# Kernel tuning notes

Measured on AMD Instinct MI355X. Metric: run time of the kernel, lower is better.

The kernel has to match this reference:

```python
import jax, jax.numpy as jnp
import numpy as np
import math

B, S, E = 2, 2048, 2048
H, KVH = 16, 4
HD = E // H  # 128
ROPE_BASE = 10000.0


def _rope_cos_sin(seq_len, dim, base=ROPE_BASE):
    inv_freq = 1.0 / (base ** (jnp.arange(0, dim, 2, dtype=jnp.float32) / dim))
    t = jnp.arange(seq_len, dtype=jnp.float32)
    freqs = jnp.outer(t, inv_freq)            # [S, dim/2]
    emb = jnp.concatenate([freqs, freqs], -1)  # [S, dim]
    return jnp.cos(emb), jnp.sin(emb)          # each [S, dim]


def _rotate_half(x):
    h = x.shape[-1] // 2
    return jnp.concatenate([-x[..., h:], x[..., :h]], axis=-1)


def setup_inputs() -> dict:
    key = jax.random.key(0)
    ks = jax.random.split(key, 6)
    x = jax.random.normal(ks[0], (B, S, E), dtype=jnp.float32)
    # xavier_uniform for Linear(in, out): weight stored as [out, in] in torch;
    # we store transposed [in, out] for x @ W.
    def xavier(k, fan_in, fan_out):
        a = math.sqrt(6.0 / (fan_in + fan_out))
        return jax.random.uniform(k, (fan_in, fan_out), jnp.float32, -a, a)
    wq = xavier(ks[1], E, H * HD)
    wk = xavier(ks[2], E, KVH * HD)
    wv = xavier(ks[3], E, KVH * HD)
    wo = xavier(ks[4], E, E)
    # causal mask: True above diagonal => masked
    attn_mask = jnp.triu(jnp.ones((S, S), dtype=bool), k=1)
    return {"x": x, "wq": wq, "wk": wk, "wv": wv, "wo": wo, "attn_mask": attn_mask}


def reference(x, wq, wk, wv, wo, attn_mask):
    b, s, _ = x.shape
    q = (x @ wq).reshape(b, s, H, HD).transpose(0, 2, 1, 3)     # [B,H,S,HD]
    k = (x @ wk).reshape(b, s, KVH, HD).transpose(0, 2, 1, 3)   # [B,KVH,S,HD]
    v = (x @ wv).reshape(b, s, KVH, HD).transpose(0, 2, 1, 3)
    cos, sin = _rope_cos_sin(s, HD)
    cos = cos[None, None]  # [1,1,S,HD]
    sin = sin[None, None]
    q = q * cos + _rotate_half(q) * sin
    k = k * cos + _rotate_half(k) * sin
    # repeat KV heads to match Q heads (GQA)
    groups = H // KVH
    k = jnp.repeat(k, groups, axis=1)  # [B,H,S,HD]
    v = jnp.repeat(v, groups, axis=1)
    scale = 1.0 / math.sqrt(HD)
    scores = jnp.einsum('bhqd,bhkd->bhqk', q, k) * scale  # [B,H,S,S]
    scores = jnp.where(attn_mask[None, None], -jnp.inf, scores)
    attn = jax.nn.softmax(scores, axis=-1)
    out = jnp.einsum('bhqk,bhkd->bhqd', attn, v)  # [B,H,S,HD]
    out = out.transpose(0, 2, 1, 3).reshape(b, s, E)
    return out @ wo
```

## Files before the change

kernel.cpp:

```cpp
#include <hip/hip_runtime.h>
#include <math.h>

#define S_LEN 2048
#define EDIM  2048
#define HDIM  128

typedef __attribute__((ext_vector_type(8))) __bf16 bf16x8;
typedef __attribute__((ext_vector_type(4))) __bf16 bf16x4;
typedef __attribute__((ext_vector_type(4))) float  f32x4;

__device__ __forceinline__ f32x4 mfma16x16x32(bf16x8 a, bf16x8 b, f32x4 c) {
  return __builtin_amdgcn_mfma_f32_16x16x32_bf16(a, b, c, 0, 0, 0);
}

__device__ __forceinline__ void gload_lds16(const __bf16* g, __bf16* l) {
  __builtin_amdgcn_global_load_lds(
      (const __attribute__((address_space(1))) void*)g,
      (__attribute__((address_space(3))) void*)l, 16, 0, 0);
}

__global__ void zero_flag(int* f) { *f = 0; }

__global__ void probe_dtype(const unsigned int* __restrict__ x, int* __restrict__ flag) {
  const int tid = threadIdx.x;
  int cnt = 0;
  for (int i = tid; i < 4096; i += 256) {
    unsigned e = (x[i] >> 7) & 0xFFu;
    cnt += (e >= 110u && e <= 135u) ? 1 : 0;
  }
  #pragma unroll
  for (int m = 1; m < 64; m <<= 1) cnt += __shfl_xor(cnt, m, 64);
  if ((tid & 63) == 0) atomicAdd(flag, cnt);
}

__global__ __launch_bounds__(256) void xconv(const void* __restrict__ xv,
                                             __bf16* __restrict__ xb,
                                             const int* __restrict__ flag) {
  const bool bf = (*flag > 2048);
  const size_t base = ((size_t)blockIdx.x * 256 + threadIdx.x) * 8;
  bf16x8 v;
  if (bf) {
    v = *(const bf16x8*)((const __bf16*)xv + base);
  } else {
    const float* xf = (const float*)xv + base;
    float4 f0 = *(const float4*)(xf);
    float4 f1 = *(const float4*)(xf + 4);
    v[0] = (__bf16)f0.x; v[1] = (__bf16)f0.y; v[2] = (__bf16)f0.z; v[3] = (__bf16)f0.w;
    v[4] = (__bf16)f1.x; v[5] = (__bf16)f1.y; v[6] = (__bf16)f1.z; v[7] = (__bf16)f1.w;
  }
  *(bf16x8*)(xb + base) = v;
}

__global__ __launch_bounds__(256) void trans_w(const void* __restrict__ Wv,
                                               __bf16* __restrict__ WT,
                                               int Kd, int Nd,
                                               const int* __restrict__ flag) {
  const bool bf = (*flag > 2048);
  __shared__ __bf16 t[64 * 72];
  const int tid = threadIdx.x;
  const int n0 = blockIdx.x * 64, k0 = blockIdx.y * 64;
  #pragma unroll
  for (int it = 0; it < 2; ++it) {
    int q = tid + it * 256;
    int r = q >> 3, c8 = q & 7;
    size_t gb = (size_t)(k0 + r) * Nd + n0 + c8 * 8;
    bf16x8 v;
    if (bf) {
      v = *(const bf16x8*)((const __bf16*)Wv + gb);
    } else {
      const float* wf = (const float*)Wv + gb;
      float4 f0 = *(const float4*)(wf);
      float4 f1 = *(const float4*)(wf + 4);
      v[0] = (__bf16)f0.x; v[1] = (__bf16)f0.y; v[2] = (__bf16)f0.z; v[3] = (__bf16)f0.w;
      v[4] = (__bf16)f1.x; v[5] = (__bf16)f1.y; v[6] = (__bf16)f1.z; v[7] = (__bf16)f1.w;
    }
    int eo = (c8 * 8) ^ (((r >> 3) & 7) * 8);
    *(bf16x8*)&t[r * 72 + eo] = v;
  }
  __syncthreads();
  #pragma unroll
  for (int it = 0; it < 2; ++it) {
    int q = tid + it * 256;
    int nl = q >> 3, kc = q & 7;
    bf16x8 o;
    #pragma unroll
    for (int i = 0; i < 8; ++i)
      o[i] = t[(kc * 8 + i) * 72 + (nl ^ (kc * 8))];
    *(bf16x8*)(WT + (size_t)(n0 + nl) * Kd + k0 + kc * 8) = o;
  }
}

__global__ __launch_bounds__(256) void trans_v(const __bf16* __restrict__ SRC,
                                               __bf16* __restrict__ VT,
                                               int str, int off) {
  __shared__ __bf16 t[64 * 72];
  const int tid = threadIdx.x;
  const int n0 = blockIdx.x * 64, k0 = blockIdx.y * 64;
  #pragma unroll
  for (int it = 0; it < 2; ++it) {
    int q = tid + it * 256;
    int r = q >> 3, c8 = q & 7;
    bf16x8 v = *(const bf16x8*)(SRC + (size_t)(k0 + r) * str + off + n0 + c8 * 8);
    int eo = (c8 * 8) ^ (((r >> 3) & 7) * 8);
    *(bf16x8*)&t[r * 72 + eo] = v;
  }
  __syncthreads();
  #pragma unroll
  for (int it = 0; it < 2; ++it) {
    int q = tid + it * 256;
    int nl = q >> 3, kc = q & 7;
    bf16x8 o;
    #pragma unroll
    for (int i = 0; i < 8; ++i)
      o[i] = t[(kc * 8 + i) * 72 + (nl ^ (kc * 8))];
    *(bf16x8*)(VT + (size_t)(n0 + nl) * 4096 + k0 + kc * 8) = o;
  }
}

__global__ __launch_bounds__(256) void gemm_tt(
    const __bf16* __restrict__ A, const __bf16* __restrict__ BT,
    void* __restrict__ Cv, int M, int N, int Kd,
    const int* __restrict__ flag, int cForceBf)
{
  const bool cbf = cForceBf || (*flag > 2048);
  __shared__ __bf16 sa[128 * 64];
  __shared__ __bf16 sb[128 * 64];
  const int tid = threadIdx.x;
  const int lane = tid & 63, w = tid >> 6;
  const int l15 = lane & 15, lg = lane >> 4;
  const int wr = w >> 1, wc = w & 1;
  const int m0 = blockIdx.y * 128, n0 = blockIdx.x * 128;
  const int lrow = lane >> 3, lcol = (lane & 7) * 8;

  f32x4 acc[4][4];
  #pragma unroll
  for (int i = 0; i < 4; ++i)
    #pragma unroll
    for (int j = 0; j < 4; ++j) acc[i][j] = (f32x4)(0.f);

  const __bf16* Ab = A + (size_t)(m0 + w * 32 + lrow) * Kd + lcol;
  const __bf16* Bb = BT + (size_t)(n0 + w * 32 + lrow) * Kd + lcol;

  for (int k0 = 0; k0 < Kd; k0 += 64) {
    __syncthreads();
    #pragma unroll
    for (int c = 0; c < 4; ++c) {
      gload_lds16(Ab + (size_t)(8 * c) * Kd + k0, &sa[(w * 4 + c) * 512]);
      gload_lds16(Bb + (size_t)(8 * c) * Kd + k0, &sb[(w * 4 + c) * 512]);
    }
    __syncthreads();
    #pragma unroll
    for (int ks = 0; ks < 2; ++ks) {
      bf16x8 af[4], bfr[4];
      #pragma unroll
      for (int i = 0; i < 4; ++i)
        af[i] = *(const bf16x8*)&sa[(wr * 64 + i * 16 + l15) * 64 + ks * 32 + lg * 8];
      #pragma unroll
      for (int j = 0; j < 4; ++j)
        bfr[j] = *(const bf16x8*)&sb[(wc * 64 + j * 16 + l15) * 64 + ks * 32 + lg * 8];
      #pragma unroll
      for (int i = 0; i < 4; ++i)
        #pragma unroll
        for (int j = 0; j < 4; ++j)
          acc[i][j] = mfma16x16x32(af[i], bfr[j], acc[i][j]);
    }
  }
  __bf16* Cb = (__bf16*)Cv;
  float*  Cf = (float*)Cv;
  #pragma unroll
  for (int i = 0; i < 4; ++i)
    #pragma unroll
    for (int j = 0; j < 4; ++j)
      #pragma unroll
      for (int r = 0; r < 4; ++r) {
        int row = m0 + wr * 64 + i * 16 + lg * 4 + r;
        int col = n0 + wc * 64 + j * 16 + l15;
        if (cbf) Cb[(size_t)row * N + col] = (__bf16)acc[i][j][r];
        else     Cf[(size_t)row * N + col] = acc[i][j][r];
      }
}

__global__ __launch_bounds__(256) void rope_bf16(__bf16* __restrict__ buf, int lognh,
                                                 int strideElems, float scale)
{
  const int idx = blockIdx.x * 256 + threadIdx.x;
  const int g   = idx & 7;
  const int h   = (idx >> 3) & ((1 << lognh) - 1);
  const int row = idx >> (3 + lognh);
  const int t   = row & (S_LEN - 1);
  __bf16* p = buf + (size_t)row * strideElems + h * HDIM + g * 8;
  bf16x8 v0 = *(bf16x8*)(p);
  bf16x8 v1 = *(bf16x8*)(p + 64);
  bf16x8 o0, o1;
  #pragma unroll
  for (int j = 0; j < 8; ++j) {
    int i = g * 8 + j;
    float inv = exp2f(-(float)i * 0.2076205059304601f);
    float ang = (float)t * inv;
    float sn, cs;
    sincosf(ang, &sn, &cs);
    cs *= scale; sn *= scale;
    float x0 = (float)v0[j], x1 = (float)v1[j];
    o0[j] = (__bf16)(x0 * cs - x1 * sn);
    o1[j] = (__bf16)(x1 * cs + x0 * sn);
  }
  *(bf16x8*)(p)      = o0;
  *(bf16x8*)(p + 64) = o1;
}

__device__ __forceinline__ void sm_fixed(
    f32x4 (&st)[4], float& l,
    __bf16* pls, int l15, int lg, int qglob, int kv0, bool diag,
    bf16x8& pa0, bf16x8& pa1)
{
  float rs = 0.f;
  #pragma unroll
  for (int kt = 0; kt < 4; ++kt) {
    bf16x4 pk;
    #pragma unroll
    for (int r = 0; r < 4; ++r) {
      float s = st[kt][r] - 16.f;
      if (diag && (kv0 + kt * 16 + lg * 4 + r > qglob)) s = -1e30f;
      float e = exp2f(s);
      rs += e;
      pk[r] = (__bf16)e;
    }
    *(bf16x4*)&pls[l15 * 72 + kt * 16 + lg * 4] = pk;
  }
  rs += __shfl_xor(rs, 16, 64);
  rs += __shfl_xor(rs, 32, 64);
  l += rs;
  pa0 = *(const bf16x8*)&pls[l15 * 72 + lg * 8];
  pa1 = *(const bf16x8*)&pls[l15 * 72 + 32 + lg * 8];
}

__global__ __launch_bounds__(256, 4) void flash_fwd(
    const __bf16* __restrict__ Q, const __bf16* __restrict__ Km,
    const __bf16* __restrict__ VT, __bf16* __restrict__ O, int qkstr)
{
  __shared__ __bf16 ks[2 * 64 * 128];
  __shared__ __bf16 vt[2 * 64 * 128];
  __shared__ __bf16 pl[4][16 * 72];
  const int id = blockIdx.x;
  const int c8b = id & 255, k = id >> 8;
  const int bh = c8b & 31, g = c8b >> 5;
  const int t = (k == 0) ? g : (k == 1) ? (15 - g) : (k == 2) ? (16 + g) : (31 - g);
  const int b  = bh >> 4, h = bh & 15;
  const int kvh = h >> 2;
  const int tid = threadIdx.x;
  const int lane = tid & 63, w = tid >> 6;
  const int l15 = lane & 15, lg = lane >> 4;
  const int q0 = t * 64 + w * 16;
  const int rbase = tid >> 4, colc = tid & 15;
  const int vd = tid >> 3, vkc = tid & 7;

  const __bf16* kgb = Km + (size_t)(b * S_LEN) * qkstr + kvh * HDIM + colc * 8;
  const __bf16* vgb = VT + (size_t)(kvh * HDIM + vd) * (2 * S_LEN) + b * S_LEN + vkc * 8;

  bf16x8 aq[4];
  {
    const __bf16* qa = Q + (size_t)(b * S_LEN + q0 + l15) * qkstr + h * HDIM + lg * 8;
    #pragma unroll
    for (int c = 0; c < 4; ++c) aq[c] = *(const bf16x8*)(qa + c * 32);
  }
  f32x4 o[8];
  float l = 0.f;
  #pragma unroll
  for (int c = 0; c < 8; ++c) o[c] = (f32x4)(0.f);

  const int rswz = ((l15 & 7) << 4) ^ (((l15 >> 3) & 1) << 6);

  bf16x8 kreg[4], vreg[4];
  #pragma unroll
  for (int it = 0; it < 4; ++it) {
    kreg[it] = *(const bf16x8*)(kgb + (size_t)(rbase + it * 16) * qkstr);
    vreg[it] = *(const bf16x8*)(vgb + (size_t)(it * 32) * (2 * S_LEN));
  }

  for (int j = 0; j <= t; ++j) {
    const int kv0 = j * 64;
    const int cur = (j & 1) * 16384;
    #pragma unroll
    for (int it = 0; it < 4; ++it) {
      int krow = rbase + it * 16;
      int kbyt = ((krow * 256 + colc * 16) ^ (((krow & 7) << 4) ^ (((krow >> 3) & 1) << 6))) + cur;
      *(bf16x8*)((char*)ks + kbyt) = kreg[it];
      int vrow = vd + it * 32;
      int vbyt = ((vrow * 128 + vkc * 16) ^ ((vrow & 7) << 4)) + cur;
      *(bf16x8*)((char*)vt + vbyt) = vreg[it];
    }
    __syncthreads();
    if (j < t) {
      #pragma unroll
      for (int it = 0; it < 4; ++it) {
        kreg[it] = *(const bf16x8*)(kgb + (size_t)(kv0 + 64 + rbase + it * 16) * qkstr);
        vreg[it] = *(const bf16x8*)(vgb + (size_t)(it * 32) * (2 * S_LEN) + kv0 + 64);
      }
    }

    f32x4 st[4];
    __builtin_amdgcn_s_setprio(1);
    #pragma unroll
    for (int kt = 0; kt < 4; ++kt) {
      st[kt] = (f32x4)(0.f);
      #pragma unroll
      for (int c = 0; c < 4; ++c) {
        int byt = (((kt * 16 + l15) * 256 + c * 64 + lg * 16) ^ rswz) + cur;
        bf16x8 kf = *(const bf16x8*)((const char*)ks + byt);
        st[kt] = mfma16x16x32(kf, aq[c], st[kt]);
      }
    }
    __builtin_amdgcn_s_setprio(0);

    bf16x8 pa0, pa1;
    sm_fixed(st, l, &pl[w][0], l15, lg, q0 + l15, kv0, j == t, pa0, pa1);

    __builtin_amdgcn_s_setprio(1);
    #pragma unroll
    for (int c = 0; c < 8; ++c) {
      int d0 = c * 16 + l15;
      int byt0 = ((d0 * 128 + lg * 16) ^ ((d0 & 7) << 4)) + cur;
      int byt1 = ((d0 * 128 + lg * 16 + 64) ^ ((d0 & 7) << 4)) + cur;
      bf16x8 bv0 = *(const bf16x8*)((const char*)vt + byt0);
      bf16x8 bv1 = *(const bf16x8*)((const char*)vt + byt1);
      o[c] = mfma16x16x32(pa0, bv0, o[c]);
      o[c] = mfma16x16x32(pa1, bv1, o[c]);
    }
    __builtin_amdgcn_s_setprio(0);
  }

  float lo[4];
  #pragma unroll
  for (int r = 0; r < 4; ++r) lo[r] = __shfl(l, lg * 4 + r, 64);
  #pragma unroll
  for (int c = 0; c < 8; ++c)
    #pragma unroll
    for (int r = 0; r < 4; ++r)
      O[(size_t)(b * S_LEN + q0 + lg * 4 + r) * EDIM + h * HDIM + c * 16 + l15] =
          (__bf16)(o[c][r] / lo[r]);
}

extern "C" void kernel_launch(void* const* d_in, const int* in_sizes, int n_in,
                              void* d_out, int out_size, void* d_ws, size_t ws_size,
                              hipStream_t stream) {
  const void* x  = d_in[0];
  const void* wq = d_in[1];
  const void* wk = d_in[2];
  const void* wv = d_in[3];
  const void* wo = d_in[4];
  char* ws = (char*)d_ws;
  int*    flagp = (int*)ws;
  __bf16* QKVw = (__bf16*)(ws + 1024);
  __bf16* R4   = (__bf16*)(ws + 1024 + (24u << 20));
  __bf16* R5   = (__bf16*)(ws + 1024 + (40u << 20));
  __bf16* VwT  = R5 + (size_t)2048 * 2048;
  const float QSCALE = 1.4426950408889634f * 0.08838834764831845f;
  dim3 blk(256);
  zero_flag<<<1, 1, 0, stream>>>(flagp);
  probe_dtype<<<1, blk, 0, stream>>>((const unsigned int*)x, flagp);
  xconv<<<4096, blk, 0, stream>>>(x, R4, flagp);

  trans_w<<<dim3(32, 32), blk, 0, stream>>>(wq, R5, EDIM, EDIM, flagp);
  trans_w<<<dim3(8, 32),  blk, 0, stream>>>(wk, R5 + (size_t)2048 * 2048, EDIM, 512, flagp);
  trans_w<<<dim3(8, 32),  blk, 0, stream>>>(wv, R5 + (size_t)2560 * 2048, EDIM, 512, flagp);
  gemm_tt<<<dim3(24, 32), blk, 0, stream>>>(R4, R5, QKVw, 4096, 3072, 2048, flagp, 1);

  rope_bf16<<<2048, blk, 0, stream>>>(QKVw, 4, 3072, QSCALE);
  rope_bf16<<<512,  blk, 0, stream>>>(QKVw + 2048, 2, 3072, 1.0f);
  trans_v<<<dim3(8, 64), blk, 0, stream>>>(QKVw, VwT, 3072, 2560);

  trans_w<<<dim3(32, 32), blk, 0, stream>>>(wo, R5, EDIM, EDIM, flagp);
  flash_fwd<<<dim3(1024), blk, 0, stream>>>(QKVw, QKVw + 2048, VwT, R4, 3072);
  gemm_tt<<<dim3(16, 32), blk, 0, stream>>>(R4, R5, d_out, 4096, 2048, 2048, flagp, 0);
}
```

Measured before the change: 265.8 us.

## Double flash-attention query tile per warp and swizzle GEMM block order

The flash attention kernel now has each block process 128 query rows instead of 64, with every warp handling two 16-row query groups. Each K/V tile loaded into LDS is therefore reused for twice as many queries, and the grid is halved to 512 blocks with a reduced occupancy hint. Warps skip fully-masked KV tiles. The GEMM also remaps block IDs with an XCD-style swizzle to improve L2 locality. This raises register pressure and lowers block count, which costs parallelism and load balance.

```diff
diff --git a/kernel.cpp b/kernel.cpp
--- a/kernel.cpp
+++ b/kernel.cpp
@@ -100,7 +100,7 @@
   for (int it = 0; it < 2; ++it) {
     int q = tid + it * 256;
     int r = q >> 3, c8 = q & 7;
-    bf16x8 v = *(const bf16x8*)(SRC + (size_t)(k0 + r) * str + off + n0 + c8 * 8);
+    bf16x8 v = *(const bf16x8*)(SRC + (size_t)(k0 + r) * str + off + c8 * 8 + n0);
     int eo = (c8 * 8) ^ (((r >> 3) & 7) * 8);
     *(bf16x8*)&t[r * 72 + eo] = v;
   }
@@ -129,7 +129,10 @@
   const int lane = tid & 63, w = tid >> 6;
   const int l15 = lane & 15, lg = lane >> 4;
   const int wr = w >> 1, wc = w & 1;
-  const int m0 = blockIdx.y * 128, n0 = blockIdx.x * 128;
+  const int nwg = gridDim.x * gridDim.y;
+  const int bid = blockIdx.y * gridDim.x + blockIdx.x;
+  const int swz = (bid & 7) * (nwg >> 3) + (bid >> 3);
+  const int m0 = (swz / gridDim.x) * 128, n0 = (swz % gridDim.x) * 128;
   const int lrow = lane >> 3, lcol = (lane & 7) * 8;
 
   f32x4 acc[4][4];
@@ -234,7 +237,7 @@
   pa1 = *(const bf16x8*)&pls[l15 * 72 + 32 + lg * 8];
 }
 
-__global__ __launch_bounds__(256, 4) void flash_fwd(
+__global__ __launch_bounds__(256, 2) void flash_fwd(
     const __bf16* __restrict__ Q, const __bf16* __restrict__ Km,
     const __bf16* __restrict__ VT, __bf16* __restrict__ O, int qkstr)
 {
@@ -242,31 +245,36 @@
   __shared__ __bf16 vt[2 * 64 * 128];
   __shared__ __bf16 pl[4][16 * 72];
   const int id = blockIdx.x;
-  const int c8b = id & 255, k = id >> 8;
-  const int bh = c8b & 31, g = c8b >> 5;
-  const int t = (k == 0) ? g : (k == 1) ? (15 - g) : (k == 2) ? (16 + g) : (31 - g);
+  const int bh = id & 31;
+  const int g = (id >> 5) & 7;
+  const int kk = id >> 8;
+  const int T = (kk == 0) ? g : (15 - g);
   const int b  = bh >> 4, h = bh & 15;
   const int kvh = h >> 2;
   const int tid = threadIdx.x;
   const int lane = tid & 63, w = tid >> 6;
   const int l15 = lane & 15, lg = lane >> 4;
-  const int q0 = t * 64 + w * 16;
+  const int q0 = T * 128 + w * 32;
   const int rbase = tid >> 4, colc = tid & 15;
   const int vd = tid >> 3, vkc = tid & 7;
+  const int nj = 2 * T + 2;
 
   const __bf16* kgb = Km + (size_t)(b * S_LEN) * qkstr + kvh * HDIM + colc * 8;
   const __bf16* vgb = VT + (size_t)(kvh * HDIM + vd) * (2 * S_LEN) + b * S_LEN + vkc * 8;
 
-  bf16x8 aq[4];
+  bf16x8 aq0[4], aq1[4];
   {
     const __bf16* qa = Q + (size_t)(b * S_LEN + q0 + l15) * qkstr + h * HDIM + lg * 8;
     #pragma unroll
-    for (int c = 0; c < 4; ++c) aq[c] = *(const bf16x8*)(qa + c * 32);
-  }
-  f32x4 o[8];
-  float l = 0.f;
-  #pragma unroll
-  for (int c = 0; c < 8; ++c) o[c] = (f32x4)(0.f);
+    for (int c = 0; c < 4; ++c) {
+      aq0[c] = *(const bf16x8*)(qa + c * 32);
+      aq1[c] = *(const bf16x8*)(qa + (size_t)16 * qkstr + c * 32);
+    }
+  }
+  f32x4 o0[8], o1[8];
+  float l0 = 0.f, l1 = 0.f;
+  #pragma unroll
+  for (int c = 0; c < 8; ++c) { o0[c] = (f32x4)(0.f); o1[c] = (f32x4)(0.f); }
 
   const int rswz = ((l15 & 7) << 4) ^ (((l15 >> 3) & 1) << 6);
 
@@ -277,7 +285,7 @@
     vreg[it] = *(const bf16x8*)(vgb + (size_t)(it * 32) * (2 * S_LEN));
   }
 
-  for (int j = 0; j <= t; ++j) {
+  for (int j = 0; j < nj; ++j) {
     const int kv0 = j * 64;
     const int cur = (j & 1) * 16384;
     #pragma unroll
@@ -290,7 +298,7 @@
       *(bf16x8*)((char*)vt + vbyt) = vreg[it];
     }
     __syncthreads();
-    if (j < t) {
+    if (j < nj - 1) {
       #pragma unroll
       for (int it = 0; it < 4; ++it) {
         kreg[it] = *(const bf16x8*)(kgb + (size_t)(kv0 + 64 + rbase + it * 16) * qkstr);
@@ -298,46 +306,59 @@
       }
     }
 
-    f32x4 st[4];
-    __builtin_amdgcn_s_setprio(1);
-    #pragma unroll
-    for (int kt = 0; kt < 4; ++kt) {
-      st[kt] = (f32x4)(0.f);
-      #pragma unroll
-      for (int c = 0; c < 4; ++c) {
-        int byt = (((kt * 16 + l15) * 256 + c * 64 + lg * 16) ^ rswz) + cur;
-        bf16x8 kf = *(const bf16x8*)((const char*)ks + byt);
-        st[kt] = mfma16x16x32(kf, aq[c], st[kt]);
+    if (kv0 <= q0 + 31) {
+      f32x4 st0[4], st1[4];
+      __builtin_amdgcn_s_setprio(1);
+      #pragma unroll
+      for (int kt = 0; kt < 4; ++kt) {
+        st0[kt] = (f32x4)(0.f);
+        st1[kt] = (f32x4)(0.f);
+        #pragma unroll
+        for (int c = 0; c < 4; ++c) {
+          int byt = (((kt * 16 + l15) * 256 + c * 64 + lg * 16) ^ rswz) + cur;
+          bf16x8 kf = *(const bf16x8*)((const char*)ks + byt);
+          st0[kt] = mfma16x16x32(kf, aq0[c], st0[kt]);
+          st1[kt] = mfma16x16x32(kf, aq1[c], st1[kt]);
+        }
       }
-    }
-    __builtin_amdgcn_s_setprio(0);
-
-    bf16x8 pa0, pa1;
-    sm_fixed(st, l, &pl[w][0], l15, lg, q0 + l15, kv0, j == t, pa0, pa1);
-
-    __builtin_amdgcn_s_setprio(1);
-    #pragma unroll
-    for (int c = 0; c < 8; ++c) {
-      int d0 = c * 16 + l15;
-      int byt0 = ((d0 * 128 + lg * 16) ^ ((d0 & 7) << 4)) + cur;
-      int byt1 = ((d0 * 128 + lg * 16 + 64) ^ ((d0 & 7) << 4)) + cur;
-      bf16x8 bv0 = *(const bf16x8*)((const char*)vt + byt0);
-      bf16x8 bv1 = *(const bf16x8*)((const char*)vt + byt1);
-      o[c] = mfma16x16x32(pa0, bv0, o[c]);
-      o[c] = mfma16x16x32(pa1, bv1, o[c]);
-    }
-    __builtin_amdgcn_s_setprio(0);
-  }
-
-  float lo[4];
-  #pragma unroll
-  for (int r = 0; r < 4; ++r) lo[r] = __shfl(l, lg * 4 + r, 64);
+      __builtin_amdgcn_s_setprio(0);
+
+      bf16x8 pa00, pa01, pa10, pa11;
+      sm_fixed(st0, l0, &pl[w][0], l15, lg, q0 + l15, kv0, kv0 + 63 > q0, pa00, pa01);
+      sm_fixed(st1, l1, &pl[w][0], l15, lg, q0 + 16 + l15, kv0, kv0 + 63 > q0 + 16, pa10, pa11);
+
+      __builtin_amdgcn_s_setprio(1);
+      #pragma unroll
+      for (int c = 0; c < 8; ++c) {
+        int d0 = c * 16 + l15;
+        int byt0 = ((d0 * 128 + lg * 16) ^ ((d0 & 7) << 4)) + cur;
+        int byt1 = ((d0 * 128 + lg * 16 + 64) ^ ((d0 & 7) << 4)) + cur;
+        bf16x8 bv0 = *(const bf16x8*)((const char*)vt + byt0);
+        bf16x8 bv1 = *(const bf16x8*)((const char*)vt + byt1);
+        o0[c] = mfma16x16x32(pa00, bv0, o0[c]);
+        o0[c] = mfma16x16x32(pa01, bv1, o0[c]);
+        o1[c] = mfma16x16x32(pa10, bv0, o1[c]);
+        o1[c] = mfma16x16x32(pa11, bv1, o1[c]);
+      }
+      __builtin_amdgcn_s_setprio(0);
+    }
+  }
+
+  float lo0[4], lo1[4];
+  #pragma unroll
+  for (int r = 0; r < 4; ++r) {
+    lo0[r] = __shfl(l0, lg * 4 + r, 64);
+    lo1[r] = __shfl(l1, lg * 4 + r, 64);
+  }
   #pragma unroll
   for (int c = 0; c < 8; ++c)
     #pragma unroll
-    for (int r = 0; r < 4; ++r)
+    for (int r = 0; r < 4; ++r) {
       O[(size_t)(b * S_LEN + q0 + lg * 4 + r) * EDIM + h * HDIM + c * 16 + l15] =
-          (__bf16)(o[c][r] / lo[r]);
+          (__bf16)(o0[c][r] / lo0[r]);
+      O[(size_t)(b * S_LEN + q0 + 16 + lg * 4 + r) * EDIM + h * HDIM + c * 16 + l15] =
+          (__bf16)(o1[c][r] / lo1[r]);
+    }
 }
 
 extern "C" void kernel_launch(void* const* d_in, const int* in_sizes, int n_in,
@@ -354,6 +375,7 @@
   __bf16* R4   = (__bf16*)(ws + 1024 + (24u << 20));
   __bf16* R5   = (__bf16*)(ws + 1024 + (40u << 20));
   __bf16* VwT  = R5 + (size_t)2048 * 2048;
+
   const float QSCALE = 1.4426950408889634f * 0.08838834764831845f;
   dim3 blk(256);
   zero_flag<<<1, 1, 0, stream>>>(flagp);
@@ -370,6 +392,6 @@
   trans_v<<<dim3(8, 64), blk, 0, stream>>>(QKVw, VwT, 3072, 2560);
 
   trans_w<<<dim3(32, 32), blk, 0, stream>>>(wo, R5, EDIM, EDIM, flagp);
-  flash_fwd<<<dim3(1024), blk, 0, stream>>>(QKVw, QKVw + 2048, VwT, R4, 3072);
+  flash_fwd<<<dim3(512), blk, 0, stream>>>(QKVw, QKVw + 2048, VwT, R4, 3072);
   gemm_tt<<<dim3(16, 32), blk, 0, stream>>>(R4, R5, d_out, 4096, 2048, 2048, flagp, 0);
 }
```

After: 288.3 us. 8.5% more time.
